# Optimization experiments

Measured on AMD Instinct MI355X. Metric: run time of the kernel, lower is better.

## Reference

```python
import jax, jax.numpy as jnp
import numpy as np

B, S, D, T = 512, 65536, 256, 10   # graphs, substructures, emb_dim, num_tasks
THRESHOLD = 0.4                    # CausalGNN threshold default
MEMBER_P = 0.002                   # ~131 substructures per graph


def setup_inputs() -> dict:
    key = jax.random.key(0)
    ks = jax.random.split(key, 8)
    def w(k, shape):
        fan_in = shape[0]
        return jax.random.normal(k, shape, jnp.float32) / np.float32(np.sqrt(fan_in))
    return {
        "h_graph": jax.random.normal(ks[0], (B, D), jnp.float32),
        "h_sub":   jax.random.normal(ks[1], (S, D), jnp.float32),
        "W1": w(ks[2], (D, 2 * D)),  "b1": jnp.zeros((2 * D,), jnp.float32),
        "W2": w(ks[3], (2 * D, 1)),  "b2": jnp.zeros((1,), jnp.float32),
        "Wc": w(ks[4], (2 * D, T)),  "bc": jnp.zeros((T,), jnp.float32),
        # dense [B,S] bool membership: mask[i,j] = substructure j belongs to graph i
        "mask": jax.random.bernoulli(ks[5], MEMBER_P, (B, S)),
    }


def _l2_normalize(x, eps=1e-12):  # F.normalize(p=2, dim=1)
    n = jnp.linalg.norm(x, axis=1, keepdims=True)
    return x / jnp.maximum(n, eps)


def reference(h_graph, h_sub, W1, b1, W2, b2, Wc, bc, mask):
    # SubMaskGenerator: Linear -> ReLU -> Dropout(eval=identity) -> Linear -> sigmoid, squeeze
    gate_logits = (jax.nn.relu(h_sub @ W1 + b1) @ W2 + b2)[:, 0]      # [S]
    subgraph_mask = jax.nn.sigmoid(gate_logits)                        # [S]

    # fused masked segment mean (replaces per-graph python loop + host sync):
    # valid[i,j] = (sub j in graph i) & (gate > threshold)
    valid = mask & (subgraph_mask > THRESHOLD)                         # [B,S] bool
    w = valid.astype(h_sub.dtype)
    counts = w.sum(axis=1, keepdims=True)                              # [B,1]
    sums = w @ h_sub                                                   # [B,D]
    h_sub_aligned = jnp.where(counts > 0, sums / jnp.maximum(counts, 1.0), 0.0)

    h_sub_norm = _l2_normalize(h_sub_aligned)
    h_graph_norm = _l2_normalize(h_graph)
    # F.cosine_similarity(dim=1, eps=1e-8) on the already-normalized vectors
    na = jnp.linalg.norm(h_sub_norm, axis=1)
    ng = jnp.linalg.norm(h_graph_norm, axis=1)
    cos = (h_sub_norm * h_graph_norm).sum(axis=1) / (
        jnp.maximum(na, 1e-8) * jnp.maximum(ng, 1e-8))
    cosine_loss = 1.0 - cos.mean()

    h_combined = jnp.concatenate([h_graph, h_sub_aligned], axis=1)     # [B,2D]
    logits = h_combined @ Wc + bc                                      # [B,T]
    return logits, cosine_loss, subgraph_mask
```

## Files before the change

### kernel.cpp

```cpp
#include <hip/hip_runtime.h>
#include <math.h>

#define D 256
#define H 512
#define TT 10
#define THRESH 0.4f
#define KS 8
#define NSPLIT 8

typedef __attribute__((ext_vector_type(8))) _Float16 half8;
typedef __attribute__((ext_vector_type(4))) float f32x4;

__global__ __launch_bounds__(256) void w1_prep(const float* __restrict__ W1,
                                               short* __restrict__ W1s)
{
    const int tid = blockIdx.x * 256 + threadIdx.x;
    const int lane = tid & 63;
    const int cell = tid >> 6;
    const int k = cell & 7;
    const int n = cell >> 3;
    const int row0 = k * 32 + (lane >> 4) * 8;
    const int col = n * 16 + (lane & 15);
    _Float16 h8[8];
    #pragma unroll
    for (int i = 0; i < 8; ++i)
        h8[i] = (_Float16)W1[(size_t)(row0 + i) * H + col];
    *reinterpret_cast<half8*>(W1s + (((size_t)n * 8 + k) * 64 + lane) * 8) =
        *reinterpret_cast<half8*>(h8);
}

__global__ __launch_bounds__(256, 2) void gate_mfma(
    const float* __restrict__ h_sub,
    const short* __restrict__ W1s,
    const float* __restrict__ b1,
    const float* __restrict__ W2,
    const float* __restrict__ b2,
    float* __restrict__ submask,
    unsigned* __restrict__ gbits)
{
    __shared__ __align__(16) short sW[4][2][4096];
    __shared__ float sb1[H], sw2[H];
    const int tid = threadIdx.x;
    const int lane = tid & 63;
    const int w = tid >> 6;
    const int base = blockIdx.x * 128 + w * 32;
    const int rot = (blockIdx.x * 4 + w) & 31;
    const float bb = b2[0];

    {
        int i = tid * 2;
        *reinterpret_cast<float2*>(&sb1[i]) = *reinterpret_cast<const float2*>(&b1[i]);
        *reinterpret_cast<float2*>(&sw2[i]) = *reinterpret_cast<const float2*>(&W2[i]);
    }

    half8 af[2][KS];
    #pragma unroll
    for (int s = 0; s < 2; ++s) {
        const int row = base + s * 16 + (lane & 15);
        const float* rp = h_sub + (size_t)row * D + (lane >> 4) * 8;
        #pragma unroll
        for (int k = 0; k < KS; ++k) {
            float x[8];
            *reinterpret_cast<float4*>(&x[0]) =
                *reinterpret_cast<const float4*>(rp + k * 32);
            *reinterpret_cast<float4*>(&x[4]) =
                *reinterpret_cast<const float4*>(rp + k * 32 + 4);
            _Float16 h8[8];
            #pragma unroll
            for (int i = 0; i < 8; ++i) h8[i] = (_Float16)x[i];
            af[s][k] = *reinterpret_cast<half8*>(h8);
        }
    }

    __syncthreads();

    auto stage = [&](int c, int b) {
        const char* gp = (const char*)W1s + ((size_t)(c & 31) << 13)
                       + (size_t)lane * 16;
        char* lp0 = (char*)&sW[w][b][0] + lane * 16;
        #pragma unroll
        for (int i = 0; i < 8; ++i) {
            __builtin_amdgcn_global_load_lds(
                (const __attribute__((address_space(1))) void*)(gp + i * 1024),
                (__attribute__((address_space(3))) void*)(lp0 + i * 1024),
                16, 0, 0);
        }
    };

    stage(rot, 0);
    stage(rot + 1, 1);

    float lp[2][4] = {{0.f,0.f,0.f,0.f},{0.f,0.f,0.f,0.f}};

    for (int cc = 0; cc < 32; ++cc) {
        if (cc < 31) asm volatile("s_waitcnt vmcnt(8)" ::: "memory");
        else         asm volatile("s_waitcnt vmcnt(0)" ::: "memory");
        __builtin_amdgcn_sched_barrier(0);

        const int c = (cc + rot) & 31;
        const short* buf = &sW[w][cc & 1][0];
        f32x4 acc[2];
        acc[0] = (f32x4){0.f,0.f,0.f,0.f};
        acc[1] = (f32x4){0.f,0.f,0.f,0.f};

        #pragma unroll
        for (int k = 0; k < KS; ++k) {
            half8 bh = *reinterpret_cast<const half8*>(buf + (k * 64 + lane) * 8);
            acc[0] = __builtin_amdgcn_mfma_f32_16x16x32_f16(af[0][k], bh, acc[0], 0, 0, 0);
            acc[1] = __builtin_amdgcn_mfma_f32_16x16x32_f16(af[1][k], bh, acc[1], 0, 0, 0);
        }

        const int h = c * 16 + (lane & 15);
        const float b1h = sb1[h], w2h = sw2[h];
        #pragma unroll
        for (int s = 0; s < 2; ++s)
            #pragma unroll
            for (int j = 0; j < 4; ++j) {
                float v = acc[s][j] + b1h;
                v = v > 0.f ? v : 0.f;
                lp[s][j] = fmaf(v, w2h, lp[s][j]);
            }

        __builtin_amdgcn_sched_barrier(0);
        if (cc < 30) stage(cc + rot + 2, cc & 1);
    }

    #pragma unroll
    for (int m = 1; m < 16; m <<= 1)
        #pragma unroll
        for (int s = 0; s < 2; ++s)
            #pragma unroll
            for (int j = 0; j < 4; ++j)
                lp[s][j] += __shfl_xor(lp[s][j], m);

    const int g = lane >> 4;
    unsigned bits = 0;
    float sig[2][4];
    #pragma unroll
    for (int s = 0; s < 2; ++s)
        #pragma unroll
        for (int j = 0; j < 4; ++j) {
            sig[s][j] = 1.f / (1.f + expf(-(lp[s][j] + bb)));
            if (sig[s][j] > THRESH) bits |= 1u << (s * 16 + g * 4 + j);
        }
    bits |= __shfl_xor(bits, 16);
    bits |= __shfl_xor(bits, 32);
    if (lane == 0) gbits[blockIdx.x * 4 + w] = bits;

    if ((lane & 15) == 0)
        #pragma unroll
        for (int s = 0; s < 2; ++s)
            #pragma unroll
            for (int j = 0; j < 4; ++j)
                submask[base + s * 16 + g * 4 + j] = sig[s][j];
}

__global__ __launch_bounds__(256) void seg_scan(
    const float* __restrict__ h_sub,
    const int*   __restrict__ mask,
    const unsigned* __restrict__ gbits,
    float* __restrict__ psum,
    int*   __restrict__ pcnt,
    int S)
{
    const int i = blockIdx.x / NSPLIT;
    const int p = blockIdx.x % NSPLIT;
    const int tid = threadIdx.x;
    const int lane = tid & 63;
    const int w = tid >> 6;
    const int seg = S / NSPLIT;
    const int start = p * seg;
    const int* mrow = mask + (size_t)i * S + start;

    __shared__ unsigned sbits[8192 / 32];
    {
        const int nw = seg / 32;
        for (int t = tid; t < nw; t += 256) sbits[t] = gbits[(start >> 5) + t];
    }
    __syncthreads();

    float4 acc = make_float4(0.f, 0.f, 0.f, 0.f);
    int cnt = 0;

    const int per = seg / 4;
    for (int base = w * per; base < (w + 1) * per; base += 256) {
        const int j0 = base + (lane << 2);
        int4 m4 = *reinterpret_cast<const int4*>(mrow + j0);
        const unsigned bw = sbits[j0 >> 5];
        const int sh = j0 & 31;
        unsigned long long bal[4];
        bal[0] = __ballot((m4.x != 0) & ((bw >> (sh + 0)) & 1u));
        bal[1] = __ballot((m4.y != 0) & ((bw >> (sh + 1)) & 1u));
        bal[2] = __ballot((m4.z != 0) & ((bw >> (sh + 2)) & 1u));
        bal[3] = __ballot((m4.w != 0) & ((bw >> (sh + 3)) & 1u));
        #pragma unroll
        for (int s = 0; s < 4; ++s) {
            unsigned long long b = bal[s];
            while (b) {
                int t = __builtin_ctzll(b);
                b &= b - 1;
                int jj = start + base + (t << 2) + s;
                float4 hv = *reinterpret_cast<const float4*>(
                    h_sub + (size_t)jj * D + (lane << 2));
                acc.x += hv.x; acc.y += hv.y; acc.z += hv.z; acc.w += hv.w;
                cnt++;
            }
        }
    }

    __shared__ float ssum[4][D];
    __shared__ int   scnt[4];
    *reinterpret_cast<float4*>(&ssum[w][lane << 2]) = acc;
    if (lane == 0) scnt[w] = cnt;
    __syncthreads();

    float a = ssum[0][tid] + ssum[1][tid] + ssum[2][tid] + ssum[3][tid];
    psum[(size_t)blockIdx.x * D + tid] = a;
    if (tid == 0) pcnt[blockIdx.x] = scnt[0] + scnt[1] + scnt[2] + scnt[3];
}

__global__ __launch_bounds__(256) void seg_combine(
    const float* __restrict__ h_graph,
    const float* __restrict__ psum,
    const int*   __restrict__ pcnt,
    const float* __restrict__ Wc,
    const float* __restrict__ bc,
    float* __restrict__ logits,
    float* __restrict__ cos_ws)
{
    const int i = blockIdx.x;
    const int tid = threadIdx.x;
    const int lane = tid & 63;
    const int w = tid >> 6;

    float a = 0.f;
    int c = 0;
    #pragma unroll
    for (int p = 0; p < NSPLIT; ++p) {
        a += psum[((size_t)i * NSPLIT + p) * D + tid];
        c += pcnt[i * NSPLIT + p];
    }
    a = (c > 0) ? (a / (float)c) : 0.f;
    const float g = h_graph[(size_t)i * D + tid];

    float r0 = a * a, r1 = g * g, r2 = a * g;
    #pragma unroll
    for (int m = 1; m < 64; m <<= 1) {
        r0 += __shfl_xor(r0, m);
        r1 += __shfl_xor(r1, m);
        r2 += __shfl_xor(r2, m);
    }
    __shared__ float red[4][3];
    if (lane == 0) { red[w][0] = r0; red[w][1] = r1; red[w][2] = r2; }
    __syncthreads();
    if (tid == 0) {
        float a2 = red[0][0] + red[1][0] + red[2][0] + red[3][0];
        float g2 = red[0][1] + red[1][1] + red[2][1] + red[3][1];
        float ag = red[0][2] + red[1][2] + red[2][2] + red[3][2];
        float an = sqrtf(a2), gn = sqrtf(g2);
        float cs = (c > 0) ? (ag / (fmaxf(an, 1e-12f) * fmaxf(gn, 1e-12f))) : 0.f;
        cos_ws[i] = cs;
    }

    float lg[TT];
    #pragma unroll
    for (int t = 0; t < TT; ++t)
        lg[t] = g * Wc[(size_t)tid * TT + t] + a * Wc[(size_t)(D + tid) * TT + t];
    #pragma unroll
    for (int m = 1; m < 64; m <<= 1)
        #pragma unroll
        for (int t = 0; t < TT; ++t) lg[t] += __shfl_xor(lg[t], m);
    __shared__ float lpart[4][TT];
    if (lane == 0)
        #pragma unroll
        for (int t = 0; t < TT; ++t) lpart[w][t] = lg[t];
    __syncthreads();
    if (tid < TT)
        logits[(size_t)i * TT + tid] =
            lpart[0][tid] + lpart[1][tid] + lpart[2][tid] + lpart[3][tid] + bc[tid];
}

__global__ void loss_kernel(const float* __restrict__ cos_ws,
                            float* __restrict__ out, int B)
{
    const int lane = threadIdx.x;
    float s = 0.f;
    for (int i = lane; i < B; i += 64) s += cos_ws[i];
    #pragma unroll
    for (int m = 1; m < 64; m <<= 1) s += __shfl_xor(s, m);
    if (lane == 0) out[0] = 1.0f - s / (float)B;
}

extern "C" void kernel_launch(void* const* d_in, const int* in_sizes, int n_in,
                              void* d_out, int out_size, void* d_ws, size_t ws_size,
                              hipStream_t stream)
{
    const float* h_graph = (const float*)d_in[0];
    const float* h_sub   = (const float*)d_in[1];
    const float* W1      = (const float*)d_in[2];
    const float* b1      = (const float*)d_in[3];
    const float* W2      = (const float*)d_in[4];
    const float* b2      = (const float*)d_in[5];
    const float* Wc      = (const float*)d_in[6];
    const float* bc      = (const float*)d_in[7];
    const int*   mask    = (const int*)d_in[8];

    const int B = in_sizes[0] / D;
    const int S = in_sizes[1] / D;

    float* out     = (float*)d_out;
    float* logits  = out;
    float* loss    = out + (size_t)B * TT;
    float* submask = loss + 1;

    char* ws = (char*)d_ws;
    short*    W1s    = (short*)ws;
    unsigned* gbits  = (unsigned*)(ws + 512 * 1024);
    int*      pcnt   = (int*)(ws + 528 * 1024);
    float*    cos_ws = (float*)(ws + 560 * 1024);
    float*    psum   = (float*)(ws + 1024 * 1024);

    w1_prep<<<64, 256, 0, stream>>>(W1, W1s);
    gate_mfma<<<S / 128, 256, 0, stream>>>(h_sub, W1s, b1, W2, b2, submask, gbits);
    seg_scan<<<B * NSPLIT, 256, 0, stream>>>(h_sub, mask, gbits, psum, pcnt, S);
    seg_combine<<<B, 256, 0, stream>>>(h_graph, psum, pcnt, Wc, bc, logits, cos_ws);
    loss_kernel<<<1, 64, 0, stream>>>(cos_ws, loss, B);
}
```

Before: 77.33 us.

## Split gate hidden dimension across wave pairs and halve LDS staging per wave

The gate kernel now assigns each 32-row group to two waves, each covering half of the 512 hidden columns. Partial logits are combined through shared memory before the sigmoid and ballot-based bitmask. Per-wave LDS staging buffers are halved by streaming half-K chunks, and launch bounds move to 4 blocks per CU with twice as many blocks. The aim is higher occupancy and shorter per-wave serial loops, in exchange for an extra block-wide sync, a cross-wave reduction, and duplicated loads of the h_sub fragments per wave pair.

```diff
diff --git a/kernel.cpp b/kernel.cpp
--- a/kernel.cpp
+++ b/kernel.cpp
@@ -29,7 +29,7 @@
         *reinterpret_cast<half8*>(h8);
 }
 
-__global__ __launch_bounds__(256, 2) void gate_mfma(
+__global__ __launch_bounds__(256, 4) void gate_mfma(
     const float* __restrict__ h_sub,
     const short* __restrict__ W1s,
     const float* __restrict__ b1,
@@ -38,13 +38,16 @@
     float* __restrict__ submask,
     unsigned* __restrict__ gbits)
 {
-    __shared__ __align__(16) short sW[4][2][4096];
+    __shared__ __align__(16) short sW[4][2][2048];
     __shared__ float sb1[H], sw2[H];
+    __shared__ float red[2][2][32];
     const int tid = threadIdx.x;
     const int lane = tid & 63;
     const int w = tid >> 6;
-    const int base = blockIdx.x * 128 + w * 32;
-    const int rot = (blockIdx.x * 4 + w) & 31;
+    const int half = w & 1;
+    const int r = w >> 1;
+    const int base = blockIdx.x * 64 + r * 32;
+    const int rotn = (blockIdx.x + 5 * w) & 15;
     const float bb = b2[0];
 
     {
@@ -74,12 +77,14 @@
 
     __syncthreads();
 
-    auto stage = [&](int c, int b) {
-        const char* gp = (const char*)W1s + ((size_t)(c & 31) << 13)
+    auto ntile = [&](int j) { return half * 16 + ((j + rotn) & 15); };
+    auto stage = [&](int s, int b) {
+        const int n = ntile(s >> 1), kk = s & 1;
+        const char* gp = (const char*)W1s + (size_t)n * 8192 + (size_t)kk * 4096
                        + (size_t)lane * 16;
         char* lp0 = (char*)&sW[w][b][0] + lane * 16;
         #pragma unroll
-        for (int i = 0; i < 8; ++i) {
+        for (int i = 0; i < 4; ++i) {
             __builtin_amdgcn_global_load_lds(
                 (const __attribute__((address_space(1))) void*)(gp + i * 1024),
                 (__attribute__((address_space(3))) void*)(lp0 + i * 1024),
@@ -87,72 +92,75 @@
         }
     };
 
-    stage(rot, 0);
-    stage(rot + 1, 1);
+    stage(0, 0);
+    stage(1, 1);
 
     float lp[2][4] = {{0.f,0.f,0.f,0.f},{0.f,0.f,0.f,0.f}};
-
-    for (int cc = 0; cc < 32; ++cc) {
-        if (cc < 31) asm volatile("s_waitcnt vmcnt(8)" ::: "memory");
-        else         asm volatile("s_waitcnt vmcnt(0)" ::: "memory");
+    f32x4 acc[2];
+
+    for (int s = 0; s < 32; ++s) {
+        if (s < 31) asm volatile("s_waitcnt vmcnt(4)" ::: "memory");
+        else        asm volatile("s_waitcnt vmcnt(0)" ::: "memory");
         __builtin_amdgcn_sched_barrier(0);
 
-        const int c = (cc + rot) & 31;
-        const short* buf = &sW[w][cc & 1][0];
-        f32x4 acc[2];
-        acc[0] = (f32x4){0.f,0.f,0.f,0.f};
-        acc[1] = (f32x4){0.f,0.f,0.f,0.f};
-
-        #pragma unroll
-        for (int k = 0; k < KS; ++k) {
+        const int kk = s & 1;
+        if (kk == 0) {
+            acc[0] = (f32x4){0.f,0.f,0.f,0.f};
+            acc[1] = (f32x4){0.f,0.f,0.f,0.f};
+        }
+        const short* buf = &sW[w][s & 1][0];
+        #pragma unroll
+        for (int k = 0; k < 4; ++k) {
             half8 bh = *reinterpret_cast<const half8*>(buf + (k * 64 + lane) * 8);
-            acc[0] = __builtin_amdgcn_mfma_f32_16x16x32_f16(af[0][k], bh, acc[0], 0, 0, 0);
-            acc[1] = __builtin_amdgcn_mfma_f32_16x16x32_f16(af[1][k], bh, acc[1], 0, 0, 0);
-        }
-
-        const int h = c * 16 + (lane & 15);
-        const float b1h = sb1[h], w2h = sw2[h];
-        #pragma unroll
-        for (int s = 0; s < 2; ++s)
+            acc[0] = __builtin_amdgcn_mfma_f32_16x16x32_f16(af[0][kk * 4 + k], bh, acc[0], 0, 0, 0);
+            acc[1] = __builtin_amdgcn_mfma_f32_16x16x32_f16(af[1][kk * 4 + k], bh, acc[1], 0, 0, 0);
+        }
+        if (kk == 1) {
+            const int hc = ntile(s >> 1) * 16 + (lane & 15);
+            const float b1h = sb1[hc], w2h = sw2[hc];
             #pragma unroll
-            for (int j = 0; j < 4; ++j) {
-                float v = acc[s][j] + b1h;
-                v = v > 0.f ? v : 0.f;
-                lp[s][j] = fmaf(v, w2h, lp[s][j]);
-            }
+            for (int t = 0; t < 2; ++t)
+                #pragma unroll
+                for (int j = 0; j < 4; ++j) {
+                    float v = acc[t][j] + b1h;
+                    v = v > 0.f ? v : 0.f;
+                    lp[t][j] = fmaf(v, w2h, lp[t][j]);
+                }
+        }
 
         __builtin_amdgcn_sched_barrier(0);
-        if (cc < 30) stage(cc + rot + 2, cc & 1);
+        if (s < 30) stage(s + 2, s & 1);
     }
 
     #pragma unroll
     for (int m = 1; m < 16; m <<= 1)
         #pragma unroll
-        for (int s = 0; s < 2; ++s)
+        for (int t = 0; t < 2; ++t)
             #pragma unroll
             for (int j = 0; j < 4; ++j)
-                lp[s][j] += __shfl_xor(lp[s][j], m);
-
-    const int g = lane >> 4;
-    unsigned bits = 0;
-    float sig[2][4];
-    #pragma unroll
-    for (int s = 0; s < 2; ++s)
-        #pragma unroll
-        for (int j = 0; j < 4; ++j) {
-            sig[s][j] = 1.f / (1.f + expf(-(lp[s][j] + bb)));
-            if (sig[s][j] > THRESH) bits |= 1u << (s * 16 + g * 4 + j);
-        }
-    bits |= __shfl_xor(bits, 16);
-    bits |= __shfl_xor(bits, 32);
-    if (lane == 0) gbits[blockIdx.x * 4 + w] = bits;
-
-    if ((lane & 15) == 0)
-        #pragma unroll
-        for (int s = 0; s < 2; ++s)
+                lp[t][j] += __shfl_xor(lp[t][j], m);
+
+    if ((lane & 15) == 0) {
+        const int g = lane >> 4;
+        #pragma unroll
+        for (int t = 0; t < 2; ++t)
             #pragma unroll
             for (int j = 0; j < 4; ++j)
-                submask[base + s * 16 + g * 4 + j] = sig[s][j];
+                red[r][half][t * 16 + g * 4 + j] = lp[t][j];
+    }
+    __syncthreads();
+
+    if (half == 0) {
+        const bool act = lane < 32;
+        float sig = 0.f;
+        if (act) {
+            float logit = red[r][0][lane] + red[r][1][lane] + bb;
+            sig = 1.f / (1.f + expf(-logit));
+        }
+        unsigned long long bal = __ballot(act && (sig > THRESH));
+        if (act) submask[base + lane] = sig;
+        if (lane == 0) gbits[blockIdx.x * 2 + r] = (unsigned)bal;
+    }
 }
 
 __global__ __launch_bounds__(256) void seg_scan(
@@ -321,7 +329,7 @@
     float*    psum   = (float*)(ws + 1024 * 1024);
 
     w1_prep<<<64, 256, 0, stream>>>(W1, W1s);
-    gate_mfma<<<S / 128, 256, 0, stream>>>(h_sub, W1s, b1, W2, b2, submask, gbits);
+    gate_mfma<<<S / 64, 256, 0, stream>>>(h_sub, W1s, b1, W2, b2, submask, gbits);
     seg_scan<<<B * NSPLIT, 256, 0, stream>>>(h_sub, mask, gbits, psum, pcnt, S);
     seg_combine<<<B, 256, 0, stream>>>(h_graph, psum, pcnt, Wc, bc, logits, cos_ws);
     loss_kernel<<<1, 64, 0, stream>>>(cos_ws, loss, B);
```

Measured after the change: 208.0 us. +169.0%, slower.

## Share half of W1 in LDS across 8 waves, stage second half via registers

Applied to the files above, without the earlier changes.

The gate kernel now runs 512-thread blocks over 256 rows. Each block loads the first half of the fp16 W1 (128 KB) into shared LDS and prefetches the second half into registers while the first half is consumed, then swaps it in after a barrier. This replaces the old scheme where each wave streamed its own double-buffered W1 chunks, so the block issues fewer global W1 loads. In exchange it uses a large LDS footprint that limits occupancy to one block per CU, adds 16 float4 staging registers per thread, and serialises the two halves with barriers.

```diff
diff --git a/kernel.cpp b/kernel.cpp
--- a/kernel.cpp
+++ b/kernel.cpp
@@ -29,7 +29,7 @@
         *reinterpret_cast<half8*>(h8);
 }
 
-__global__ __launch_bounds__(256, 2) void gate_mfma(
+__global__ __launch_bounds__(512) void gate_mfma(
     const float* __restrict__ h_sub,
     const short* __restrict__ W1s,
     const float* __restrict__ b1,
@@ -38,20 +38,27 @@
     float* __restrict__ submask,
     unsigned* __restrict__ gbits)
 {
-    __shared__ __align__(16) short sW[4][2][4096];
+    __shared__ __align__(16) short sB[65536];
     __shared__ float sb1[H], sw2[H];
     const int tid = threadIdx.x;
     const int lane = tid & 63;
     const int w = tid >> 6;
-    const int base = blockIdx.x * 128 + w * 32;
-    const int rot = (blockIdx.x * 4 + w) & 31;
+    const int base = blockIdx.x * 256 + w * 32;
     const float bb = b2[0];
 
     {
-        int i = tid * 2;
-        *reinterpret_cast<float2*>(&sb1[i]) = *reinterpret_cast<const float2*>(&b1[i]);
-        *reinterpret_cast<float2*>(&sw2[i]) = *reinterpret_cast<const float2*>(&W2[i]);
-    }
+        const char* gp = (const char*)W1s + (size_t)tid * 16;
+        char* lp0 = (char*)sB + (size_t)tid * 16;
+        #pragma unroll
+        for (int i = 0; i < 16; ++i) {
+            __builtin_amdgcn_global_load_lds(
+                (const __attribute__((address_space(1))) void*)(gp + i * 8192),
+                (__attribute__((address_space(3))) void*)(lp0 + i * 8192),
+                16, 0, 0);
+        }
+    }
+    sb1[tid] = b1[tid];
+    sw2[tid] = W2[tid];
 
     half8 af[2][KS];
     #pragma unroll
@@ -74,85 +81,103 @@
 
     __syncthreads();
 
-    auto stage = [&](int c, int b) {
-        const char* gp = (const char*)W1s + ((size_t)(c & 31) << 13)
-                       + (size_t)lane * 16;
-        char* lp0 = (char*)&sW[w][b][0] + lane * 16;
-        #pragma unroll
-        for (int i = 0; i < 8; ++i) {
-            __builtin_amdgcn_global_load_lds(
-                (const __attribute__((address_space(1))) void*)(gp + i * 1024),
-                (__attribute__((address_space(3))) void*)(lp0 + i * 1024),
-                16, 0, 0);
-        }
-    };
-
-    stage(rot, 0);
-    stage(rot + 1, 1);
+    float4 stg[16];
+    {
+        const float4* p1 = reinterpret_cast<const float4*>(
+                               (const char*)W1s + 131072) + tid;
+        #pragma unroll
+        for (int i = 0; i < 16; ++i) stg[i] = p1[i * 512];
+    }
 
     float lp[2][4] = {{0.f,0.f,0.f,0.f},{0.f,0.f,0.f,0.f}};
 
-    for (int cc = 0; cc < 32; ++cc) {
-        if (cc < 31) asm volatile("s_waitcnt vmcnt(8)" ::: "memory");
-        else         asm volatile("s_waitcnt vmcnt(0)" ::: "memory");
-        __builtin_amdgcn_sched_barrier(0);
-
-        const int c = (cc + rot) & 31;
-        const short* buf = &sW[w][cc & 1][0];
-        f32x4 acc[2];
-        acc[0] = (f32x4){0.f,0.f,0.f,0.f};
-        acc[1] = (f32x4){0.f,0.f,0.f,0.f};
-
+    #pragma unroll
+    for (int nn = 0; nn < 16; ++nn) {
+        const int n = (nn + w) & 15;
+        f32x4 acc0 = (f32x4){0.f,0.f,0.f,0.f};
+        f32x4 acc1 = (f32x4){0.f,0.f,0.f,0.f};
         #pragma unroll
         for (int k = 0; k < KS; ++k) {
-            half8 bh = *reinterpret_cast<const half8*>(buf + (k * 64 + lane) * 8);
-            acc[0] = __builtin_amdgcn_mfma_f32_16x16x32_f16(af[0][k], bh, acc[0], 0, 0, 0);
-            acc[1] = __builtin_amdgcn_mfma_f32_16x16x32_f16(af[1][k], bh, acc[1], 0, 0, 0);
-        }
-
-        const int h = c * 16 + (lane & 15);
-        const float b1h = sb1[h], w2h = sw2[h];
-        #pragma unroll
-        for (int s = 0; s < 2; ++s)
-            #pragma unroll
-            for (int j = 0; j < 4; ++j) {
-                float v = acc[s][j] + b1h;
-                v = v > 0.f ? v : 0.f;
-                lp[s][j] = fmaf(v, w2h, lp[s][j]);
-            }
-
-        __builtin_amdgcn_sched_barrier(0);
-        if (cc < 30) stage(cc + rot + 2, cc & 1);
+            half8 bh = *reinterpret_cast<const half8*>(
+                sB + ((n * 8 + k) * 64 + lane) * 8);
+            acc0 = __builtin_amdgcn_mfma_f32_16x16x32_f16(af[0][k], bh, acc0, 0, 0, 0);
+            acc1 = __builtin_amdgcn_mfma_f32_16x16x32_f16(af[1][k], bh, acc1, 0, 0, 0);
+        }
+        const int hc = n * 16 + (lane & 15);
+        const float b1h = sb1[hc], w2h = sw2[hc];
+        #pragma unroll
+        for (int j = 0; j < 4; ++j) {
+            float v0 = acc0[j] + b1h;
+            v0 = v0 > 0.f ? v0 : 0.f;
+            lp[0][j] = fmaf(v0, w2h, lp[0][j]);
+            float v1 = acc1[j] + b1h;
+            v1 = v1 > 0.f ? v1 : 0.f;
+            lp[1][j] = fmaf(v1, w2h, lp[1][j]);
+        }
+    }
+
+    __syncthreads();
+
+    {
+        float4* dst = reinterpret_cast<float4*>(sB) + tid;
+        #pragma unroll
+        for (int i = 0; i < 16; ++i) dst[i * 512] = stg[i];
+    }
+    __syncthreads();
+
+    #pragma unroll
+    for (int nn = 0; nn < 16; ++nn) {
+        const int n = (nn + w) & 15;
+        f32x4 acc0 = (f32x4){0.f,0.f,0.f,0.f};
+        f32x4 acc1 = (f32x4){0.f,0.f,0.f,0.f};
+        #pragma unroll
+        for (int k = 0; k < KS; ++k) {
+            half8 bh = *reinterpret_cast<const half8*>(
+                sB + ((n * 8 + k) * 64 + lane) * 8);
+            acc0 = __builtin_amdgcn_mfma_f32_16x16x32_f16(af[0][k], bh, acc0, 0, 0, 0);
+            acc1 = __builtin_amdgcn_mfma_f32_16x16x32_f16(af[1][k], bh, acc1, 0, 0, 0);
+        }
+        const int hc = 256 + n * 16 + (lane & 15);
+        const float b1h = sb1[hc], w2h = sw2[hc];
+        #pragma unroll
+        for (int j = 0; j < 4; ++j) {
+            float v0 = acc0[j] + b1h;
+            v0 = v0 > 0.f ? v0 : 0.f;
+            lp[0][j] = fmaf(v0, w2h, lp[0][j]);
+            float v1 = acc1[j] + b1h;
+            v1 = v1 > 0.f ? v1 : 0.f;
+            lp[1][j] = fmaf(v1, w2h, lp[1][j]);
+        }
     }
 
     #pragma unroll
     for (int m = 1; m < 16; m <<= 1)
         #pragma unroll
-        for (int s = 0; s < 2; ++s)
+        for (int t = 0; t < 2; ++t)
             #pragma unroll
             for (int j = 0; j < 4; ++j)
-                lp[s][j] += __shfl_xor(lp[s][j], m);
+                lp[t][j] += __shfl_xor(lp[t][j], m);
 
     const int g = lane >> 4;
     unsigned bits = 0;
     float sig[2][4];
     #pragma unroll
-    for (int s = 0; s < 2; ++s)
+    for (int t = 0; t < 2; ++t)
         #pragma unroll
         for (int j = 0; j < 4; ++j) {
-            sig[s][j] = 1.f / (1.f + expf(-(lp[s][j] + bb)));
-            if (sig[s][j] > THRESH) bits |= 1u << (s * 16 + g * 4 + j);
+            sig[t][j] = 1.f / (1.f + expf(-(lp[t][j] + bb)));
+            if (sig[t][j] > THRESH) bits |= 1u << (t * 16 + g * 4 + j);
         }
     bits |= __shfl_xor(bits, 16);
     bits |= __shfl_xor(bits, 32);
-    if (lane == 0) gbits[blockIdx.x * 4 + w] = bits;
+    if (lane == 0) gbits[blockIdx.x * 8 + w] = bits;
 
     if ((lane & 15) == 0)
         #pragma unroll
-        for (int s = 0; s < 2; ++s)
+        for (int t = 0; t < 2; ++t)
             #pragma unroll
             for (int j = 0; j < 4; ++j)
-                submask[base + s * 16 + g * 4 + j] = sig[s][j];
+                submask[base + t * 16 + g * 4 + j] = sig[t][j];
 }
 
 __global__ __launch_bounds__(256) void seg_scan(
@@ -321,7 +346,7 @@
     float*    psum   = (float*)(ws + 1024 * 1024);
 
     w1_prep<<<64, 256, 0, stream>>>(W1, W1s);
-    gate_mfma<<<S / 128, 256, 0, stream>>>(h_sub, W1s, b1, W2, b2, submask, gbits);
+    gate_mfma<<<S / 256, 512, 0, stream>>>(h_sub, W1s, b1, W2, b2, submask, gbits);
     seg_scan<<<B * NSPLIT, 256, 0, stream>>>(h_sub, mask, gbits, psum, pcnt, S);
     seg_combine<<<B, 256, 0, stream>>>(h_graph, psum, pcnt, Wc, bc, logits, cos_ws);
     loss_kernel<<<1, 64, 0, stream>>>(cos_ws, loss, B);
```

Measured after the change: 80.03 us. 3.5% more time.

## Stage W1 in two block-shared LDS halves and give each wave 64 rows

Applied to the files above, without the earlier changes.

The gate kernel now has each block cooperatively stage half of the fp16 W1 (128KB) into shared LDS, where every wave reads it, in place of per-wave double-buffered streaming of 8KB chunks. Each wave handles 64 rows (4 MFMA row tiles) instead of 32, so every B-fragment loaded from LDS feeds four MFMAs, and the grid is halved. Stage-to-LDS traffic is shared across waves, but occupancy drops to one block per CU. The second W1 half is loaded only after a barrier, so that load is exposed rather than overlapped, and s_setprio is added around the MFMA bursts.

```diff
diff --git a/kernel.cpp b/kernel.cpp
--- a/kernel.cpp
+++ b/kernel.cpp
@@ -29,7 +29,7 @@
         *reinterpret_cast<half8*>(h8);
 }
 
-__global__ __launch_bounds__(256, 2) void gate_mfma(
+__global__ __launch_bounds__(256, 1) void gate_mfma(
     const float* __restrict__ h_sub,
     const short* __restrict__ W1s,
     const float* __restrict__ b1,
@@ -38,24 +38,33 @@
     float* __restrict__ submask,
     unsigned* __restrict__ gbits)
 {
-    __shared__ __align__(16) short sW[4][2][4096];
+    __shared__ __align__(16) short sB[65536];
     __shared__ float sb1[H], sw2[H];
     const int tid = threadIdx.x;
     const int lane = tid & 63;
     const int w = tid >> 6;
-    const int base = blockIdx.x * 128 + w * 32;
-    const int rot = (blockIdx.x * 4 + w) & 31;
+    const int base = blockIdx.x * 256 + w * 64;
     const float bb = b2[0];
 
-    {
-        int i = tid * 2;
-        *reinterpret_cast<float2*>(&sb1[i]) = *reinterpret_cast<const float2*>(&b1[i]);
-        *reinterpret_cast<float2*>(&sw2[i]) = *reinterpret_cast<const float2*>(&W2[i]);
-    }
-
-    half8 af[2][KS];
-    #pragma unroll
-    for (int s = 0; s < 2; ++s) {
+    auto stagePhase = [&](int p) {
+        const char* gp = (const char*)W1s + (size_t)p * 131072 + (size_t)tid * 16;
+        char* lp0 = (char*)sB + (size_t)tid * 16;
+        #pragma unroll
+        for (int i = 0; i < 32; ++i) {
+            __builtin_amdgcn_global_load_lds(
+                (const __attribute__((address_space(1))) void*)(gp + i * 4096),
+                (__attribute__((address_space(3))) void*)(lp0 + i * 4096),
+                16, 0, 0);
+        }
+    };
+
+    stagePhase(0);
+    sb1[tid] = b1[tid];       sb1[tid + 256] = b1[tid + 256];
+    sw2[tid] = W2[tid];       sw2[tid + 256] = W2[tid + 256];
+
+    half8 af[4][KS];
+    #pragma unroll
+    for (int s = 0; s < 4; ++s) {
         const int row = base + s * 16 + (lane & 15);
         const float* rp = h_sub + (size_t)row * D + (lane >> 4) * 8;
         #pragma unroll
@@ -72,84 +81,84 @@
         }
     }
 
-    __syncthreads();
-
-    auto stage = [&](int c, int b) {
-        const char* gp = (const char*)W1s + ((size_t)(c & 31) << 13)
-                       + (size_t)lane * 16;
-        char* lp0 = (char*)&sW[w][b][0] + lane * 16;
-        #pragma unroll
-        for (int i = 0; i < 8; ++i) {
-            __builtin_amdgcn_global_load_lds(
-                (const __attribute__((address_space(1))) void*)(gp + i * 1024),
-                (__attribute__((address_space(3))) void*)(lp0 + i * 1024),
-                16, 0, 0);
-        }
-    };
-
-    stage(rot, 0);
-    stage(rot + 1, 1);
-
-    float lp[2][4] = {{0.f,0.f,0.f,0.f},{0.f,0.f,0.f,0.f}};
-
-    for (int cc = 0; cc < 32; ++cc) {
-        if (cc < 31) asm volatile("s_waitcnt vmcnt(8)" ::: "memory");
-        else         asm volatile("s_waitcnt vmcnt(0)" ::: "memory");
-        __builtin_amdgcn_sched_barrier(0);
-
-        const int c = (cc + rot) & 31;
-        const short* buf = &sW[w][cc & 1][0];
-        f32x4 acc[2];
-        acc[0] = (f32x4){0.f,0.f,0.f,0.f};
-        acc[1] = (f32x4){0.f,0.f,0.f,0.f};
-
-        #pragma unroll
-        for (int k = 0; k < KS; ++k) {
-            half8 bh = *reinterpret_cast<const half8*>(buf + (k * 64 + lane) * 8);
-            acc[0] = __builtin_amdgcn_mfma_f32_16x16x32_f16(af[0][k], bh, acc[0], 0, 0, 0);
-            acc[1] = __builtin_amdgcn_mfma_f32_16x16x32_f16(af[1][k], bh, acc[1], 0, 0, 0);
-        }
-
-        const int h = c * 16 + (lane & 15);
-        const float b1h = sb1[h], w2h = sw2[h];
-        #pragma unroll
-        for (int s = 0; s < 2; ++s)
-            #pragma unroll
-            for (int j = 0; j < 4; ++j) {
-                float v = acc[s][j] + b1h;
-                v = v > 0.f ? v : 0.f;
-                lp[s][j] = fmaf(v, w2h, lp[s][j]);
+    float lp[4][4];
+    #pragma unroll
+    for (int s = 0; s < 4; ++s)
+        #pragma unroll
+        for (int j = 0; j < 4; ++j) lp[s][j] = 0.f;
+
+    #pragma unroll
+    for (int p = 0; p < 2; ++p) {
+        __syncthreads();
+
+        #pragma unroll
+        for (int nn = 0; nn < 16; ++nn) {
+            const int n = (nn + w * 4) & 15;
+            f32x4 acc[4];
+            #pragma unroll
+            for (int s = 0; s < 4; ++s) acc[s] = (f32x4){0.f,0.f,0.f,0.f};
+
+            __builtin_amdgcn_s_setprio(1);
+            #pragma unroll
+            for (int k = 0; k < KS; ++k) {
+                half8 bh = *reinterpret_cast<const half8*>(
+                    sB + ((n * 8 + k) * 64 + lane) * 8);
+                acc[0] = __builtin_amdgcn_mfma_f32_16x16x32_f16(af[0][k], bh, acc[0], 0, 0, 0);
+                acc[1] = __builtin_amdgcn_mfma_f32_16x16x32_f16(af[1][k], bh, acc[1], 0, 0, 0);
+                acc[2] = __builtin_amdgcn_mfma_f32_16x16x32_f16(af[2][k], bh, acc[2], 0, 0, 0);
+                acc[3] = __builtin_amdgcn_mfma_f32_16x16x32_f16(af[3][k], bh, acc[3], 0, 0, 0);
             }
-
-        __builtin_amdgcn_sched_barrier(0);
-        if (cc < 30) stage(cc + rot + 2, cc & 1);
+            __builtin_amdgcn_s_setprio(0);
+
+            const int hc = p * 256 + n * 16 + (lane & 15);
+            const float b1h = sb1[hc], w2h = sw2[hc];
+            #pragma unroll
+            for (int s = 0; s < 4; ++s)
+                #pragma unroll
+                for (int j = 0; j < 4; ++j) {
+                    float v = acc[s][j] + b1h;
+                    v = v > 0.f ? v : 0.f;
+                    lp[s][j] = fmaf(v, w2h, lp[s][j]);
+                }
+        }
+
+        if (p == 0) {
+            __syncthreads();
+            stagePhase(1);
+        }
     }
 
     #pragma unroll
     for (int m = 1; m < 16; m <<= 1)
         #pragma unroll
-        for (int s = 0; s < 2; ++s)
+        for (int s = 0; s < 4; ++s)
             #pragma unroll
             for (int j = 0; j < 4; ++j)
                 lp[s][j] += __shfl_xor(lp[s][j], m);
 
     const int g = lane >> 4;
-    unsigned bits = 0;
-    float sig[2][4];
-    #pragma unroll
-    for (int s = 0; s < 2; ++s)
+    unsigned b0 = 0, b1w = 0;
+    float sig[4][4];
+    #pragma unroll
+    for (int s = 0; s < 4; ++s)
         #pragma unroll
         for (int j = 0; j < 4; ++j) {
             sig[s][j] = 1.f / (1.f + expf(-(lp[s][j] + bb)));
-            if (sig[s][j] > THRESH) bits |= 1u << (s * 16 + g * 4 + j);
-        }
-    bits |= __shfl_xor(bits, 16);
-    bits |= __shfl_xor(bits, 32);
-    if (lane == 0) gbits[blockIdx.x * 4 + w] = bits;
-
+            const int r = s * 16 + g * 4 + j;
+            if (sig[s][j] > THRESH) {
+                if (r < 32) b0 |= 1u << r;
+                else        b1w |= 1u << (r - 32);
+            }
+        }
+    b0  |= __shfl_xor(b0, 16);  b0  |= __shfl_xor(b0, 32);
+    b1w |= __shfl_xor(b1w, 16); b1w |= __shfl_xor(b1w, 32);
+    if (lane == 0) {
+        gbits[blockIdx.x * 8 + w * 2 + 0] = b0;
+        gbits[blockIdx.x * 8 + w * 2 + 1] = b1w;
+    }
     if ((lane & 15) == 0)
         #pragma unroll
-        for (int s = 0; s < 2; ++s)
+        for (int s = 0; s < 4; ++s)
             #pragma unroll
             for (int j = 0; j < 4; ++j)
                 submask[base + s * 16 + g * 4 + j] = sig[s][j];
@@ -321,7 +330,7 @@
     float*    psum   = (float*)(ws + 1024 * 1024);
 
     w1_prep<<<64, 256, 0, stream>>>(W1, W1s);
-    gate_mfma<<<S / 128, 256, 0, stream>>>(h_sub, W1s, b1, W2, b2, submask, gbits);
+    gate_mfma<<<S / 256, 256, 0, stream>>>(h_sub, W1s, b1, W2, b2, submask, gbits);
     seg_scan<<<B * NSPLIT, 256, 0, stream>>>(h_sub, mask, gbits, psum, pcnt, S);
     seg_combine<<<B, 256, 0, stream>>>(h_graph, psum, pcnt, Wc, bc, logits, cos_ws);
     loss_kernel<<<1, 64, 0, stream>>>(cos_ws, loss, B);
```

Measured after the change: 76.12 us. No clear change (-1.6%).
